# Kernel tuning notes

Hardware: AMD Instinct MI355X
Metric: run time of the kernel (lower is better)

The kernel has to match this reference:

```python
import jax, jax.numpy as jnp
import numpy as np

N_ATOMS = 65536
N_BONDS = 98304
N_MOLS = 4096
D_IN = 128
D = 256  # d_e = d_v = d_u
REPEAT = 3


def setup_inputs() -> dict:
    key = jax.random.key(0)
    ks = jax.random.split(key, 12)
    atoms = jax.random.normal(ks[0], (N_ATOMS, D_IN), dtype=jnp.float32)
    bond_orders = jax.random.uniform(ks[1], (N_BONDS,), dtype=jnp.float32)
    bond_src = jax.random.randint(ks[2], (N_BONDS,), 0, N_ATOMS, dtype=jnp.int32)
    bond_dst = jax.random.randint(ks[3], (N_BONDS,), 0, N_ATOMS, dtype=jnp.int32)
    atom_mol = jnp.sort(jax.random.randint(ks[4], (N_ATOMS,), 0, N_MOLS, dtype=jnp.int32))
    bond_mol = jnp.sort(jax.random.randint(ks[5], (N_BONDS,), 0, N_MOLS, dtype=jnp.int32))
    def w(k, fan_in, fan_out):
        return jax.random.normal(k, (fan_in, fan_out), dtype=jnp.float32) / np.sqrt(fan_in)
    W_fe = w(ks[6], 1, D)
    W_fv = w(ks[7], D_IN, D)
    W_fu = w(ks[8], D_IN, D)
    W_e = w(ks[9], 5 * D, D)   # [h_e, h_e0, h_left, h_right, u_e]
    W_v = w(ks[10], 4 * D, D)  # [h_v, h_v0, e_bar_v, u_v]
    W_u = w(ks[11], 4 * D, D)  # [h_u, h_u0, e_bar, v_bar]
    return {"atoms": atoms, "bond_orders": bond_orders, "bond_src": bond_src,
            "bond_dst": bond_dst, "atom_mol": atom_mol, "bond_mol": bond_mol,
            "W_fe": W_fe, "W_fv": W_fv, "W_fu": W_fu,
            "W_e": W_e, "W_v": W_v, "W_u": W_u}


def _graphnet(atoms, bond_orders, bond_src, bond_dst, atom_mol, bond_mol,
              W_fe, W_fv, W_fu, W_e, W_v, W_u):
    seg_sum = lambda x, ids: jax.ops.segment_sum(x, ids, num_segments=N_MOLS)
    # f_e / f_v: initial edge / node embeddings
    h_e0 = jnp.tanh(bond_orders[:, None] @ W_fe)          # [n_bonds, D]
    h_v0 = jnp.tanh(atoms @ W_fv)                          # [n_atoms, D]
    # f_u: per-molecule mean of raw atom features -> global embedding
    counts = seg_sum(jnp.ones((atoms.shape[0], 1), atoms.dtype), atom_mol)
    mol_mean = seg_sum(atoms, atom_mol) / jnp.maximum(counts, 1.0)
    h_u0 = jnp.tanh(mol_mean @ W_fu)                       # [n_mols, D]

    def step(carry, _):
        h_e, h_v, h_u = carry
        # pairwise_update is identity (default) -> per-mol loop is a no-op
        h_left = h_v[bond_src]                             # gather endpoints
        h_right = h_v[bond_dst]
        u_e = h_u[bond_mol]                                # global attr per edge
        h_e = jnp.tanh(jnp.concatenate([h_e, h_e0, h_left, h_right, u_e], axis=1) @ W_e)
        # rho_e_v: sum edge updates into both endpoint atoms
        e_bar_v = jnp.zeros_like(h_v).at[bond_src].add(h_e).at[bond_dst].add(h_e)
        u_v = h_u[atom_mol]                                # global attr per atom
        h_v = jnp.tanh(jnp.concatenate([h_v, h_v0, e_bar_v, u_v], axis=1) @ W_v)
        # rho_e_u / rho_v_u: per-molecule segment sums
        e_bar = seg_sum(h_e, bond_mol)
        v_bar = seg_sum(h_v, atom_mol)
        h_u = jnp.tanh(jnp.concatenate([h_u, h_u0, e_bar, v_bar], axis=1) @ W_u)
        return (h_e, h_v, h_u), None

    (h_e, h_v, h_u), _ = jax.lax.scan(step, (h_e0, h_v0, h_u0), None, length=REPEAT)
    # f_r default returns its first argument: the final edge representation
    return h_e


def reference(atoms, bond_orders, bond_src, bond_dst, atom_mol, bond_mol,
              W_fe, W_fv, W_fu, W_e, W_v, W_u):
    return _graphnet(atoms, bond_orders, bond_src, bond_dst, atom_mol, bond_mol,
                     W_fe, W_fv, W_fu, W_e, W_v, W_u)
```

## Files before the change

### kernel.cpp

```cpp
#include <hip/hip_runtime.h>
#include <cstdint>
#include <cmath>

#define N_ATOMS 65536
#define N_BONDS 98304
#define N_MOLS  4096
#define D_IN    128
#define DD      256
#define REPEAT  3

typedef __attribute__((ext_vector_type(8))) short short8;
typedef __attribute__((ext_vector_type(4))) float f32x4;
typedef unsigned short ushort_t;

__device__ __forceinline__ unsigned short f2h(float f) {
  union { _Float16 h; unsigned short u; } x; x.h = (_Float16)f; return x.u;
}
__device__ __forceinline__ float h2f(unsigned short u) {
  union { unsigned short u; _Float16 h; } x; x.u = u; return (float)x.h;
}

#define GLD16(gp, lp) __builtin_amdgcn_global_load_lds( \
    (const __attribute__((address_space(1))) void*)(gp), \
    (__attribute__((address_space(3))) void*)(lp), 16, 0, 0)

template<int NSEG, int SEGW, int BM>
__global__ __launch_bounds__(BM * 4)
void mfma_concat_gemm(const ushort_t* __restrict__ s0, const int* __restrict__ i0,
                      const ushort_t* __restrict__ s1, const int* __restrict__ i1,
                      const ushort_t* __restrict__ s2, const int* __restrict__ i2,
                      const ushort_t* __restrict__ s3, const int* __restrict__ i3,
                      const ushort_t* __restrict__ s4, const int* __restrict__ i4,
                      const ushort_t* __restrict__ Wt,
                      ushort_t* __restrict__ ob, ushort_t* __restrict__ ob2,
                      float* __restrict__ of)
{
  constexpr int NT     = BM * 4;
  constexpr int KW     = NSEG * SEGW;
  constexpr int SPS    = SEGW / 32;
  constexpr int ABYTES = BM * 64;
  constexpr int TILE   = ABYTES + 16384;
  constexpr int BI     = 16384 / (NT * 16);

  __shared__ __align__(16) char smem[2 * TILE];

  const int t      = threadIdx.x;
  const int m0     = blockIdx.x * BM;
  const int srcoff = (((t & 3) ^ ((t >> 2) & 3) ^ ((t >> 4) & 3)) << 4);
  const int toff   = t * 16;

  const char* arows[5];
  {
    const int rg = m0 + (t >> 2);
    const int* ips[5] = { i0, i1, i2, i3, i4 };
    const ushort_t* sps[5] = { s0, s1, s2, s3, s4 };
    #pragma unroll
    for (int s = 0; s < NSEG; ++s) {
      int idx = ips[s] ? ips[s][rg] : rg;
      arows[s] = (const char*)sps[s] + (size_t)idx * (SEGW * 2);
    }
  }

  const char* wtb[4];
  #pragma unroll
  for (int i = 0; i < BI; ++i)
    wtb[i] = (const char*)Wt + (size_t)((i * (NT >> 2) + (t >> 2)) * KW) * 2 + srcoff;

  f32x4 acc[4][4];
  const f32x4 z = {0.f, 0.f, 0.f, 0.f};
  #pragma unroll
  for (int a = 0; a < 4; ++a)
    #pragma unroll
    for (int b = 0; b < 4; ++b) acc[a][b] = z;

  const int l   = t & 63;
  const int wid = t >> 6;
  const int wr  = wid >> 2;
  const int wc  = wid & 3;
  const int swz = (((l >> 4) ^ (l & 3) ^ ((l >> 2) & 3)) << 4);
  const int aro = wr * 4096 + (l & 15) * 64 + swz;
  const int bro = ABYTES + wc * 4096 + (l & 15) * 64 + swz;

  auto stage_tile = [&](int segS, int sub, int db) {
    GLD16(arows[segS] + sub * 64 + srcoff, smem + db + toff);
    const int kt = segS * SPS + sub;
    #pragma unroll
    for (int i = 0; i < BI; ++i)
      GLD16(wtb[i] + (size_t)kt * 64, smem + db + ABYTES + i * (NT * 16) + toff);
  };
  auto compute = [&](int sb) {
    short8 af[4], bfv[4];
    #pragma unroll
    for (int mf = 0; mf < 4; ++mf) af[mf]  = *(const short8*)(smem + sb + aro + mf * 1024);
    #pragma unroll
    for (int nf = 0; nf < 4; ++nf) bfv[nf] = *(const short8*)(smem + sb + bro + nf * 1024);
    #pragma unroll
    for (int mf = 0; mf < 4; ++mf)
      #pragma unroll
      for (int nf = 0; nf < 4; ++nf)
        acc[mf][nf] = __builtin_amdgcn_mfma_f32_16x16x32_f16(af[mf], bfv[nf], acc[mf][nf], 0, 0, 0);
  };

  stage_tile(0, 0, 0);
  __syncthreads();

  int cur = 0;
  #pragma unroll
  for (int seg = 0; seg < NSEG; ++seg) {
    for (int sub = 0; sub < SPS; ++sub) {
      const int nb = (cur ^ 1) * TILE;
      if (sub + 1 < SPS)            stage_tile(seg, sub + 1, nb);
      else if (seg + 1 < NSEG)      stage_tile(seg + 1, 0, nb);
      compute(cur * TILE);
      __syncthreads();
      cur ^= 1;
    }
  }

  const int colb = wc * 64 + (l & 15);
  const int rowb = m0 + wr * 64 + ((l >> 4) << 2);
  #pragma unroll
  for (int mf = 0; mf < 4; ++mf) {
    #pragma unroll
    for (int nf = 0; nf < 4; ++nf) {
      f32x4 d = acc[mf][nf];
      #pragma unroll
      for (int r = 0; r < 4; ++r) {
        float v = tanhf(d[r]);
        size_t o = (size_t)(rowb + mf * 16 + r) * DD + colb + nf * 16;
        unsigned short hv16 = f2h(v);
        ob[o] = hv16;
        if (ob2) ob2[o] = hv16;
        if (of)  of[o]  = v;
      }
    }
  }
}


__global__ __launch_bounds__(256)
void f32_to_f16(const float* __restrict__ in, ushort_t* __restrict__ out, int n4) {
  int t = blockIdx.x * 256 + threadIdx.x;
  if (t >= n4) return;
  float4 v = ((const float4*)in)[t];
  ushort4 o; o.x = f2h(v.x); o.y = f2h(v.y); o.z = f2h(v.z); o.w = f2h(v.w);
  ((ushort4*)out)[t] = o;
}

__global__ __launch_bounds__(256)
void transpose_w(const float* __restrict__ in, ushort_t* __restrict__ out, int K) {
  int t = blockIdx.x * 256 + threadIdx.x;
  int n = t / K, k = t - n * K;
  out[t] = f2h(in[(size_t)k * DD + n]);
}

__global__ __launch_bounds__(256)
void init_he0_k(const float* __restrict__ bo, const float* __restrict__ wfe,
                ushort_t* __restrict__ he0, ushort_t* __restrict__ he) {
  int t = blockIdx.x * 256 + threadIdx.x;
  int b = t >> 6, c = (t & 63) << 2;
  float o = bo[b];
  float4 w = *(const float4*)&wfe[c];
  ushort4 v;
  v.x = f2h(tanhf(o * w.x)); v.y = f2h(tanhf(o * w.y));
  v.z = f2h(tanhf(o * w.z)); v.w = f2h(tanhf(o * w.w));
  size_t idx = ((size_t)b * DD + c) >> 2;
  ((ushort4*)he0)[idx] = v; ((ushort4*)he)[idx] = v;
}

__global__ __launch_bounds__(128)
void mol_accum_sorted(const float* __restrict__ atoms, const int* __restrict__ amol,
                      float* __restrict__ msum, float* __restrict__ cnt) {
  __shared__ int sid[64];
  int r0 = blockIdx.x * 64;
  int c  = threadIdx.x;
  if (c < 64) sid[c] = amol[r0 + c];
  __syncthreads();
  float acc = 0.f; int prev = sid[0]; int run = 0;
  const float* p = atoms + (size_t)r0 * D_IN + c;
  for (int r = 0; r < 64; ++r, p += D_IN) {
    int id = sid[r];
    if (id != prev) {
      unsafeAtomicAdd(&msum[(size_t)prev * D_IN + c], acc);
      if (c == 0) unsafeAtomicAdd(&cnt[prev], (float)run);
      acc = 0.f; run = 0; prev = id;
    }
    acc += *p; run += 1;
  }
  unsafeAtomicAdd(&msum[(size_t)prev * D_IN + c], acc);
  if (c == 0) unsafeAtomicAdd(&cnt[prev], (float)run);
}

__global__ __launch_bounds__(256)
void mol_mean_h(const float* __restrict__ msum, const float* __restrict__ cnt,
                ushort_t* __restrict__ mmean) {
  int t = blockIdx.x * 256 + threadIdx.x;
  int m = t >> 5, c = (t & 31) << 2;
  float inv = 1.0f / fmaxf(cnt[m], 1.0f);
  float4 v = *(const float4*)&msum[(size_t)m * D_IN + c];
  ushort4 o; o.x = f2h(v.x * inv); o.y = f2h(v.y * inv);
  o.z = f2h(v.z * inv); o.w = f2h(v.w * inv);
  ((ushort4*)mmean)[((size_t)m * D_IN + c) >> 2] = o;
}


__global__ __launch_bounds__(256)
void count_deg(const int* __restrict__ src, const int* __restrict__ dst,
               int* __restrict__ deg) {
  int b = blockIdx.x * 256 + threadIdx.x;
  if (b >= N_BONDS) return;
  atomicAdd(&deg[src[b]], 1);
  atomicAdd(&deg[dst[b]], 1);
}

__global__ __launch_bounds__(256)
void scan_deg(const int* __restrict__ deg, int* __restrict__ rowptr,
              int* __restrict__ cursor) {
  __shared__ int partial[256];
  int t = threadIdx.x;
  int base = t * 256;
  int s = 0;
  for (int i = 0; i < 256; ++i) s += deg[base + i];
  partial[t] = s;
  __syncthreads();
  if (t == 0) {
    int acc = 0;
    for (int i = 0; i < 256; ++i) { int v = partial[i]; partial[i] = acc; acc += v; }
    rowptr[N_ATOMS] = acc;
  }
  __syncthreads();
  int acc = partial[t];
  for (int i = 0; i < 256; ++i) {
    rowptr[base + i] = acc; cursor[base + i] = acc;
    acc += deg[base + i];
  }
}

__global__ __launch_bounds__(256)
void fill_csr(const int* __restrict__ src, const int* __restrict__ dst,
              int* __restrict__ cursor, int* __restrict__ list) {
  int b = blockIdx.x * 256 + threadIdx.x;
  if (b >= N_BONDS) return;
  int p = atomicAdd(&cursor[src[b]], 1); list[p] = b;
  int q = atomicAdd(&cursor[dst[b]], 1); list[q] = b;
}

__global__ __launch_bounds__(256)
void gather_ebv(const ushort_t* __restrict__ he, const int* __restrict__ rowptr,
                const int* __restrict__ list, ushort_t* __restrict__ ebv_h) {
  int t = blockIdx.x * 256 + threadIdx.x;
  int a = t >> 6, c = (t & 63) << 2;
  int s = rowptr[a], e = rowptr[a + 1];
  float a0 = 0.f, a1 = 0.f, a2 = 0.f, a3 = 0.f;
  for (int i = s; i < e; ++i) {
    int b = list[i];
    ushort4 v = *(const ushort4*)&he[(size_t)b * DD + c];
    a0 += h2f(v.x); a1 += h2f(v.y); a2 += h2f(v.z); a3 += h2f(v.w);
  }
  ushort4 o; o.x = f2h(a0); o.y = f2h(a1); o.z = f2h(a2); o.w = f2h(a3);
  ((ushort4*)ebv_h)[((size_t)a * DD + c) >> 2] = o;
}

__global__ __launch_bounds__(256)
void seg_sum_sorted(const ushort_t* __restrict__ x, const int* __restrict__ ids,
                    float* __restrict__ out) {
  __shared__ int sid[64];
  int r0 = blockIdx.x * 64;
  int c  = threadIdx.x;
  if (c < 64) sid[c] = ids[r0 + c];
  __syncthreads();
  float acc = 0.f; int prev = sid[0];
  const ushort_t* p = x + (size_t)r0 * DD + c;
  for (int r = 0; r < 64; ++r, p += DD) {
    int id = sid[r];
    if (id != prev) { unsafeAtomicAdd(&out[(size_t)prev * DD + c], acc); acc = 0.f; prev = id; }
    acc += h2f(*p);
  }
  unsafeAtomicAdd(&out[(size_t)prev * DD + c], acc);
}


extern "C" void kernel_launch(void* const* d_in, const int* in_sizes, int n_in,
                              void* d_out, int out_size, void* d_ws, size_t ws_size,
                              hipStream_t stream)
{
  const float* atoms       = (const float*)d_in[0];
  const float* bond_orders = (const float*)d_in[1];
  const int*   bond_src    = (const int*)d_in[2];
  const int*   bond_dst    = (const int*)d_in[3];
  const int*   atom_mol    = (const int*)d_in[4];
  const int*   bond_mol    = (const int*)d_in[5];
  const float* W_fe        = (const float*)d_in[6];
  const float* W_fv        = (const float*)d_in[7];
  const float* W_fu        = (const float*)d_in[8];
  const float* W_e         = (const float*)d_in[9];
  const float* W_v         = (const float*)d_in[10];
  const float* W_u         = (const float*)d_in[11];

  char* w = (char*)d_ws;
  auto alloc = [&](size_t bytes) { char* p = w; w += (bytes + 255) & ~(size_t)255; return p; };

  ushort_t* atoms_h  = (ushort_t*)alloc((size_t)N_ATOMS * D_IN * 2);
  ushort_t* he0  = (ushort_t*)alloc((size_t)N_BONDS * DD * 2);
  ushort_t* he   = (ushort_t*)alloc((size_t)N_BONDS * DD * 2);
  ushort_t* hv0  = (ushort_t*)alloc((size_t)N_ATOMS * DD * 2);
  ushort_t* hv   = (ushort_t*)alloc((size_t)N_ATOMS * DD * 2);
  ushort_t* hu0  = (ushort_t*)alloc((size_t)N_MOLS * DD * 2);
  ushort_t* hu   = (ushort_t*)alloc((size_t)N_MOLS * DD * 2);
  ushort_t* mmean= (ushort_t*)alloc((size_t)N_MOLS * D_IN * 2);
  ushort_t* Wte  = (ushort_t*)alloc((size_t)DD * 1280 * 2);
  ushort_t* Wtv  = (ushort_t*)alloc((size_t)DD * 1024 * 2);
  ushort_t* Wtu  = (ushort_t*)alloc((size_t)DD * 1024 * 2);
  ushort_t* Wtfv = (ushort_t*)alloc((size_t)DD * D_IN * 2);
  ushort_t* Wtfu = (ushort_t*)alloc((size_t)DD * D_IN * 2);
  float* eb_f  = (float*)alloc((size_t)N_MOLS * DD * 4);
  float* vb_f  = (float*)alloc((size_t)N_MOLS * DD * 4);
  ushort_t* ebv_h = (ushort_t*)alloc((size_t)N_ATOMS * DD * 2);
  ushort_t* eb_h  = (ushort_t*)alloc((size_t)N_MOLS * DD * 2);
  ushort_t* vb_h  = (ushort_t*)alloc((size_t)N_MOLS * DD * 2);
  float* msum = (float*)alloc((size_t)N_MOLS * D_IN * 4);
  float* cnt  = (float*)alloc((size_t)N_MOLS * 4);
  int* deg    = (int*)alloc((size_t)N_ATOMS * 4);
  int* rowptr = (int*)alloc((size_t)(N_ATOMS + 1) * 4);
  int* cursor = (int*)alloc((size_t)N_ATOMS * 4);
  int* list   = (int*)alloc((size_t)2 * N_BONDS * 4);
  if ((size_t)(w - (char*)d_ws) > ws_size) return;

  const ushort_t* NU = nullptr; const int* NI = nullptr;

  f32_to_f16<<<N_ATOMS * D_IN / 4 / 256, 256, 0, stream>>>(atoms, atoms_h, N_ATOMS * D_IN / 4);
  transpose_w<<<DD * 1280 / 256, 256, 0, stream>>>(W_e, Wte, 1280);
  transpose_w<<<DD * 1024 / 256, 256, 0, stream>>>(W_v, Wtv, 1024);
  transpose_w<<<DD * 1024 / 256, 256, 0, stream>>>(W_u, Wtu, 1024);
  transpose_w<<<DD * D_IN / 256, 256, 0, stream>>>(W_fv, Wtfv, D_IN);
  transpose_w<<<DD * D_IN / 256, 256, 0, stream>>>(W_fu, Wtfu, D_IN);
  hipMemsetAsync(deg, 0, (size_t)N_ATOMS * 4, stream);
  count_deg<<<(N_BONDS + 255) / 256, 256, 0, stream>>>(bond_src, bond_dst, deg);
  scan_deg<<<1, 256, 0, stream>>>(deg, rowptr, cursor);
  fill_csr<<<(N_BONDS + 255) / 256, 256, 0, stream>>>(bond_src, bond_dst, cursor, list);

  hipMemsetAsync(msum, 0, (size_t)(N_MOLS * D_IN + N_MOLS) * 4, stream);
  mol_accum_sorted<<<N_ATOMS / 64, 128, 0, stream>>>(atoms, atom_mol, msum, cnt);
  mol_mean_h<<<N_MOLS * 32 / 256, 256, 0, stream>>>(msum, cnt, mmean);
  init_he0_k<<<N_BONDS * 64 / 256, 256, 0, stream>>>(bond_orders, W_fe, he0, he);
  mfma_concat_gemm<1, 128, 128><<<N_ATOMS / 128, 512, 0, stream>>>(
      atoms_h, NI, NU, NI, NU, NI, NU, NI, NU, NI, Wtfv, hv0, hv, nullptr);
  mfma_concat_gemm<1, 128, 64><<<N_MOLS / 64, 256, 0, stream>>>(
      mmean, NI, NU, NI, NU, NI, NU, NI, NU, NI, Wtfu, hu0, hu, nullptr);

  for (int it = 0; it < REPEAT; ++it) {
    hipMemsetAsync(eb_f, 0, (size_t)2 * N_MOLS * DD * 4, stream);
    mfma_concat_gemm<5, 256, 128><<<N_BONDS / 128, 512, 0, stream>>>(
        he, NI, he0, NI, hv, bond_src, hv, bond_dst, hu, bond_mol,
        Wte, he, nullptr, it == REPEAT - 1 ? (float*)d_out : nullptr);
    gather_ebv<<<N_ATOMS * 64 / 256, 256, 0, stream>>>(he, rowptr, list, ebv_h);
    seg_sum_sorted<<<N_BONDS / 64, 256, 0, stream>>>(he, bond_mol, eb_f);
    mfma_concat_gemm<4, 256, 128><<<N_ATOMS / 128, 512, 0, stream>>>(
        hv, NI, hv0, NI, ebv_h, NI, hu, atom_mol, NU, NI,
        Wtv, hv, nullptr, nullptr);
    seg_sum_sorted<<<N_ATOMS / 64, 256, 0, stream>>>(hv, atom_mol, vb_f);
    f32_to_f16<<<2 * N_MOLS * DD / 4 / 256, 256, 0, stream>>>(eb_f, eb_h, 2 * N_MOLS * DD / 4);
    mfma_concat_gemm<4, 256, 64><<<N_MOLS / 64, 256, 0, stream>>>(
        hu, NI, hu0, NI, eb_h, NI, vb_h, NI, NU, NI,
        Wtu, hu, nullptr, nullptr);
  }
}
```

Before: 1.087 ms.

## Pre-pack weights into MFMA fragment layout and read B operands directly from global

Weights are pre-transformed once into a layout where each wave's MFMA B fragment is a contiguous 16-byte-per-lane load. The GEMM kernel no longer stages the weight tile through LDS and reads B fragments straight from global memory, which is expected to hit L2/cache. The A tile is staged unswizzled in fragment order, so the staging and read are conflict-free without XOR swizzling. This halves LDS traffic and footprint, which can raise occupancy, but makes B loads global-latency bound and unprefetched inside the compute loop.

Measured after the change: 1.119 ms. +3.0%, slower.

```diff
diff --git a/kernel.cpp b/kernel.cpp
--- a/kernel.cpp
+++ b/kernel.cpp
@@ -31,40 +31,35 @@
                       const ushort_t* __restrict__ s2, const int* __restrict__ i2,
                       const ushort_t* __restrict__ s3, const int* __restrict__ i3,
                       const ushort_t* __restrict__ s4, const int* __restrict__ i4,
-                      const ushort_t* __restrict__ Wt,
+                      const ushort_t* __restrict__ PreW,
                       ushort_t* __restrict__ ob, ushort_t* __restrict__ ob2,
                       float* __restrict__ of)
 {
   constexpr int NT     = BM * 4;
   constexpr int KW     = NSEG * SEGW;
+  constexpr int KTOT   = KW / 32;
   constexpr int SPS    = SEGW / 32;
   constexpr int ABYTES = BM * 64;
-  constexpr int TILE   = ABYTES + 16384;
-  constexpr int BI     = 16384 / (NT * 16);
-
-  __shared__ __align__(16) char smem[2 * TILE];
-
-  const int t      = threadIdx.x;
-  const int m0     = blockIdx.x * BM;
-  const int srcoff = (((t & 3) ^ ((t >> 2) & 3) ^ ((t >> 4) & 3)) << 4);
-  const int toff   = t * 16;
+
+  __shared__ __align__(16) char smem[2 * ABYTES];
+
+  const int t  = threadIdx.x;
+  const int m0 = blockIdx.x * BM;
+
+  const int ra  = ((t >> 6) << 4) + (t & 15);
+  const int kca = (t >> 4) & 3;
 
   const char* arows[5];
   {
-    const int rg = m0 + (t >> 2);
+    const int rg = m0 + ra;
     const int* ips[5] = { i0, i1, i2, i3, i4 };
     const ushort_t* sps[5] = { s0, s1, s2, s3, s4 };
     #pragma unroll
     for (int s = 0; s < NSEG; ++s) {
       int idx = ips[s] ? ips[s][rg] : rg;
-      arows[s] = (const char*)sps[s] + (size_t)idx * (SEGW * 2);
+      arows[s] = (const char*)sps[s] + (size_t)idx * (SEGW * 2) + kca * 16;
     }
   }
-
-  const char* wtb[4];
-  #pragma unroll
-  for (int i = 0; i < BI; ++i)
-    wtb[i] = (const char*)Wt + (size_t)((i * (NT >> 2) + (t >> 2)) * KW) * 2 + srcoff;
 
   f32x4 acc[4][4];
   const f32x4 z = {0.f, 0.f, 0.f, 0.f};
@@ -77,23 +72,21 @@
   const int wid = t >> 6;
   const int wr  = wid >> 2;
   const int wc  = wid & 3;
-  const int swz = (((l >> 4) ^ (l & 3) ^ ((l >> 2) & 3)) << 4);
-  const int aro = wr * 4096 + (l & 15) * 64 + swz;
-  const int bro = ABYTES + wc * 4096 + (l & 15) * 64 + swz;
+  const int aro = wr * 4096 + l * 16;
+  const char* pwb = (const char*)PreW + ((size_t)(wc * 4) * KTOT) * 1024 + l * 16;
 
   auto stage_tile = [&](int segS, int sub, int db) {
-    GLD16(arows[segS] + sub * 64 + srcoff, smem + db + toff);
-    const int kt = segS * SPS + sub;
-    #pragma unroll
-    for (int i = 0; i < BI; ++i)
-      GLD16(wtb[i] + (size_t)kt * 64, smem + db + ABYTES + i * (NT * 16) + toff);
+    GLD16(arows[segS] + sub * 64, smem + db + t * 16);
   };
-  auto compute = [&](int sb) {
-    short8 af[4], bfv[4];
-    #pragma unroll
-    for (int mf = 0; mf < 4; ++mf) af[mf]  = *(const short8*)(smem + sb + aro + mf * 1024);
-    #pragma unroll
-    for (int nf = 0; nf < 4; ++nf) bfv[nf] = *(const short8*)(smem + sb + bro + nf * 1024);
+  auto compute = [&](int sb, int kt) {
+    short8 bfv[4];
+    #pragma unroll
+    for (int nf = 0; nf < 4; ++nf)
+      bfv[nf] = *(const short8*)(pwb + (size_t)((nf * KTOT + kt) << 10));
+    short8 af[4];
+    #pragma unroll
+    for (int mf = 0; mf < 4; ++mf)
+      af[mf] = *(const short8*)(smem + sb + aro + mf * 1024);
     #pragma unroll
     for (int mf = 0; mf < 4; ++mf)
       #pragma unroll
@@ -108,10 +101,10 @@
   #pragma unroll
   for (int seg = 0; seg < NSEG; ++seg) {
     for (int sub = 0; sub < SPS; ++sub) {
-      const int nb = (cur ^ 1) * TILE;
-      if (sub + 1 < SPS)            stage_tile(seg, sub + 1, nb);
-      else if (seg + 1 < NSEG)      stage_tile(seg + 1, 0, nb);
-      compute(cur * TILE);
+      const int nb = (cur ^ 1) * ABYTES;
+      if (sub + 1 < SPS)       stage_tile(seg, sub + 1, nb);
+      else if (seg + 1 < NSEG) stage_tile(seg + 1, 0, nb);
+      compute(cur * ABYTES, seg * SPS + sub);
       __syncthreads();
       cur ^= 1;
     }
@@ -148,10 +141,18 @@
 }
 
 __global__ __launch_bounds__(256)
-void transpose_w(const float* __restrict__ in, ushort_t* __restrict__ out, int K) {
-  int t = blockIdx.x * 256 + threadIdx.x;
-  int n = t / K, k = t - n * K;
-  out[t] = f2h(in[(size_t)k * DD + n]);
+void prew_transform(const float* __restrict__ in, ushort_t* __restrict__ out, int KTOT) {
+  int q = blockIdx.x * 256 + threadIdx.x;
+  int c  = q & 15;
+  int kc = (q >> 4) & 3;
+  int kt = (q >> 6) % KTOT;
+  int g  = (q >> 6) / KTOT;
+  int col = g * 16 + c;
+  int k0  = kt * 32 + kc * 8;
+  ushort_t* o = out + (size_t)q * 8;
+  #pragma unroll
+  for (int j = 0; j < 8; ++j)
+    o[j] = f2h(in[(size_t)(k0 + j) * DD + col]);
 }
 
 __global__ __launch_bounds__(256)
@@ -308,11 +309,11 @@
   ushort_t* hu0  = (ushort_t*)alloc((size_t)N_MOLS * DD * 2);
   ushort_t* hu   = (ushort_t*)alloc((size_t)N_MOLS * DD * 2);
   ushort_t* mmean= (ushort_t*)alloc((size_t)N_MOLS * D_IN * 2);
-  ushort_t* Wte  = (ushort_t*)alloc((size_t)DD * 1280 * 2);
-  ushort_t* Wtv  = (ushort_t*)alloc((size_t)DD * 1024 * 2);
-  ushort_t* Wtu  = (ushort_t*)alloc((size_t)DD * 1024 * 2);
-  ushort_t* Wtfv = (ushort_t*)alloc((size_t)DD * D_IN * 2);
-  ushort_t* Wtfu = (ushort_t*)alloc((size_t)DD * D_IN * 2);
+  ushort_t* PWe  = (ushort_t*)alloc((size_t)DD * 1280 * 2);
+  ushort_t* PWv  = (ushort_t*)alloc((size_t)DD * 1024 * 2);
+  ushort_t* PWu  = (ushort_t*)alloc((size_t)DD * 1024 * 2);
+  ushort_t* PWfv = (ushort_t*)alloc((size_t)DD * D_IN * 2);
+  ushort_t* PWfu = (ushort_t*)alloc((size_t)DD * D_IN * 2);
   float* eb_f  = (float*)alloc((size_t)N_MOLS * DD * 4);
   float* vb_f  = (float*)alloc((size_t)N_MOLS * DD * 4);
   ushort_t* ebv_h = (ushort_t*)alloc((size_t)N_ATOMS * DD * 2);
@@ -329,11 +330,11 @@
   const ushort_t* NU = nullptr; const int* NI = nullptr;
 
   f32_to_f16<<<N_ATOMS * D_IN / 4 / 256, 256, 0, stream>>>(atoms, atoms_h, N_ATOMS * D_IN / 4);
-  transpose_w<<<DD * 1280 / 256, 256, 0, stream>>>(W_e, Wte, 1280);
-  transpose_w<<<DD * 1024 / 256, 256, 0, stream>>>(W_v, Wtv, 1024);
-  transpose_w<<<DD * 1024 / 256, 256, 0, stream>>>(W_u, Wtu, 1024);
-  transpose_w<<<DD * D_IN / 256, 256, 0, stream>>>(W_fv, Wtfv, D_IN);
-  transpose_w<<<DD * D_IN / 256, 256, 0, stream>>>(W_fu, Wtfu, D_IN);
+  prew_transform<<<4 * 40, 256, 0, stream>>>(W_e, PWe, 40);
+  prew_transform<<<4 * 32, 256, 0, stream>>>(W_v, PWv, 32);
+  prew_transform<<<4 * 32, 256, 0, stream>>>(W_u, PWu, 32);
+  prew_transform<<<4 * 4,  256, 0, stream>>>(W_fv, PWfv, 4);
+  prew_transform<<<4 * 4,  256, 0, stream>>>(W_fu, PWfu, 4);
   hipMemsetAsync(deg, 0, (size_t)N_ATOMS * 4, stream);
   count_deg<<<(N_BONDS + 255) / 256, 256, 0, stream>>>(bond_src, bond_dst, deg);
   scan_deg<<<1, 256, 0, stream>>>(deg, rowptr, cursor);
@@ -344,24 +345,24 @@
   mol_mean_h<<<N_MOLS * 32 / 256, 256, 0, stream>>>(msum, cnt, mmean);
   init_he0_k<<<N_BONDS * 64 / 256, 256, 0, stream>>>(bond_orders, W_fe, he0, he);
   mfma_concat_gemm<1, 128, 128><<<N_ATOMS / 128, 512, 0, stream>>>(
-      atoms_h, NI, NU, NI, NU, NI, NU, NI, NU, NI, Wtfv, hv0, hv, nullptr);
+      atoms_h, NI, NU, NI, NU, NI, NU, NI, NU, NI, PWfv, hv0, hv, nullptr);
   mfma_concat_gemm<1, 128, 64><<<N_MOLS / 64, 256, 0, stream>>>(
-      mmean, NI, NU, NI, NU, NI, NU, NI, NU, NI, Wtfu, hu0, hu, nullptr);
+      mmean, NI, NU, NI, NU, NI, NU, NI, NU, NI, PWfu, hu0, hu, nullptr);
 
   for (int it = 0; it < REPEAT; ++it) {
     hipMemsetAsync(eb_f, 0, (size_t)2 * N_MOLS * DD * 4, stream);
     mfma_concat_gemm<5, 256, 128><<<N_BONDS / 128, 512, 0, stream>>>(
         he, NI, he0, NI, hv, bond_src, hv, bond_dst, hu, bond_mol,
-        Wte, he, nullptr, it == REPEAT - 1 ? (float*)d_out : nullptr);
+        PWe, he, nullptr, it == REPEAT - 1 ? (float*)d_out : nullptr);
     gather_ebv<<<N_ATOMS * 64 / 256, 256, 0, stream>>>(he, rowptr, list, ebv_h);
     seg_sum_sorted<<<N_BONDS / 64, 256, 0, stream>>>(he, bond_mol, eb_f);
     mfma_concat_gemm<4, 256, 128><<<N_ATOMS / 128, 512, 0, stream>>>(
         hv, NI, hv0, NI, ebv_h, NI, hu, atom_mol, NU, NI,
-        Wtv, hv, nullptr, nullptr);
+        PWv, hv, nullptr, nullptr);
     seg_sum_sorted<<<N_ATOMS / 64, 256, 0, stream>>>(hv, atom_mol, vb_f);
     f32_to_f16<<<2 * N_MOLS * DD / 4 / 256, 256, 0, stream>>>(eb_f, eb_h, 2 * N_MOLS * DD / 4);
     mfma_concat_gemm<4, 256, 64><<<N_MOLS / 64, 256, 0, stream>>>(
         hu, NI, hu0, NI, eb_h, NI, vb_h, NI, NU, NI,
-        Wtu, hu, nullptr, nullptr);
-  }
-}
+        PWu, hu, nullptr, nullptr);
+  }
+}
```
